# Optimization experiments

Measured on AMD Instinct MI355X. Metric: run time of the kernel, lower is better.

The kernel has to match this reference:

```python
import jax, jax.numpy as jnp
import numpy as np

INPUT_SZ, HIDDEN_SZ, OUTPUT_SZ, NUM_LAYERS, EMBED_SZ = 128, 512, 64, 4, 16
SEQ_LEN, BATCH = 128, 256


def setup_inputs() -> dict:
    key = jax.random.key(0)
    ks = jax.random.split(key, 12)
    H, E, L = HIDDEN_SZ, EMBED_SZ, NUM_LAYERS
    s = 0.05
    inp = {
        "input": jax.random.randint(ks[0], (SEQ_LEN, BATCH), 0, INPUT_SZ),
        "embed": jax.random.normal(ks[1], (INPUT_SZ, E), jnp.float32) * s,
        # layer 0 (input dim = E), dims: [dir=2, 4H, in]
        "Wih0": jax.random.normal(ks[2], (2, 4 * H, E), jnp.float32) * s,
        "Whh0": jax.random.normal(ks[3], (2, 4 * H, H), jnp.float32) * s,
        "bih0": jax.random.normal(ks[4], (2, 4 * H), jnp.float32) * s,
        "bhh0": jax.random.normal(ks[5], (2, 4 * H), jnp.float32) * s,
        # layers 1..L-1 (input dim = 2H)
        "Wih": jax.random.normal(ks[6], (L - 1, 2, 4 * H, 2 * H), jnp.float32) * s,
        "Whh": jax.random.normal(ks[7], (L - 1, 2, 4 * H, H), jnp.float32) * s,
        "bih": jax.random.normal(ks[8], (L - 1, 2, 4 * H), jnp.float32) * s,
        "bhh": jax.random.normal(ks[9], (L - 1, 2, 4 * H), jnp.float32) * s,
        "fc_w": jax.random.normal(ks[10], (OUTPUT_SZ, 4 * L * H), jnp.float32) * s,
        "fc_b": jax.random.normal(ks[11], (OUTPUT_SZ,), jnp.float32) * s,
    }
    return inp


def _lstm_forward(tokens, embed, Wih0, Whh0, bih0, bhh0, Wih, Whh, bih, bhh, fc_w, fc_b):
    L, H = NUM_LAYERS, HIDDEN_SZ
    T, B = tokens.shape
    xs = embed[tokens]  # [T, B, E]

    def step(carry, x_t):
        h, c = carry  # each [L, 2, B, H]
        x = x_t       # [B, in_dim]
        new_h, new_c = [], []
        for l in range(L):
            Wi = Wih0 if l == 0 else Wih[l - 1]
            Wh = Whh0 if l == 0 else Whh[l - 1]
            b = (bih0 + bhh0) if l == 0 else (bih[l - 1] + bhh[l - 1])
            # both directions see the same single-timestep input (PyTorch
            # bidirectional LSTM called with seq_len=1 per step)
            gates = (jnp.einsum('bi,dgi->dbg', x, Wi)
                     + jnp.einsum('dbh,dgh->dbg', h[l], Wh)
                     + b[:, None, :])  # [2, B, 4H]
            i_g, f_g, g_g, o_g = jnp.split(gates, 4, axis=-1)
            c_new = jax.nn.sigmoid(f_g) * c[l] + jax.nn.sigmoid(i_g) * jnp.tanh(g_g)
            h_new = jax.nn.sigmoid(o_g) * jnp.tanh(c_new)  # [2, B, H]
            new_h.append(h_new)
            new_c.append(c_new)
            x = jnp.concatenate([h_new[0], h_new[1]], axis=-1)  # [B, 2H]
        return (jnp.stack(new_h), jnp.stack(new_c)), None

    h0 = jnp.zeros((L, 2, B, H), xs.dtype)
    c0 = jnp.zeros((L, 2, B, H), xs.dtype)
    (h, c), _ = jax.lax.scan(step, (h0, c0), xs)

    # PyTorch layout: [2L, B, H], layer-major / direction-minor
    h = h.reshape(2 * L, B, H)
    c = c.reshape(2 * L, B, H)
    hid = jnp.concatenate([h, c], axis=2)                 # [2L, B, 2H]
    hid = hid.transpose(1, 0, 2).reshape(B, 4 * L * H)    # cat over 2L slices on dim 1
    out = hid @ fc_w.T + fc_b
    # dropout is identity at inference
    return jax.nn.softmax(out, axis=1)


def reference(input, embed, Wih0, Whh0, bih0, bhh0, Wih, Whh, bih, bhh, fc_w, fc_b):
    return _lstm_forward(input, embed, Wih0, Whh0, bih0, bhh0, Wih, Whh, bih, bhh, fc_w, fc_b)
```

## Files before the change

### kernel.cpp

```cpp
#include <hip/hip_runtime.h>

using short8 = __attribute__((ext_vector_type(8))) short;
using f32x4  = __attribute__((ext_vector_type(4))) float;

static constexpr size_t N_WF0 = (size_t)2*32*8*3*4*512;
static constexpr size_t N_WF1 = (size_t)6*32*8*6*4*512;
static constexpr size_t N_WF  = N_WF0 + N_WF1;
static constexpr size_t N_BSE = (size_t)8*2048;
static constexpr size_t N_XPE = (size_t)128*2*256*8;
static constexpr size_t N_HBE = (size_t)2*8*64*256*8;
static constexpr size_t N_CBE = (size_t)8*256*512;
static constexpr size_t N_FCT = (size_t)8192*64;
static constexpr size_t N_FL  = (size_t)8*128;

static constexpr size_t OFF_WF = 0;
static constexpr size_t OFF_BS = OFF_WF + N_WF*2;
static constexpr size_t OFF_XP = OFF_BS + N_BSE*4;
static constexpr size_t OFF_HB = OFF_XP + N_XPE*2;
static constexpr size_t OFF_CB = OFF_HB + N_HBE*2;
static constexpr size_t OFF_HF = OFF_CB + N_CBE*4;
static constexpr size_t OFF_FC = OFF_HF + N_CBE*4;
static constexpr size_t OFF_FL = OFF_FC + N_FCT*4;
static constexpr size_t WS_NEEDED = OFF_FL + N_FL*4;

static constexpr int LDS_A   = 2*8*6*1024;
static constexpr int LDS_RED = 8*4*16*20*4;
static constexpr int LDS_C   = 16*256*4;
static constexpr int LDS_TOT = LDS_A + LDS_RED + LDS_C;

__device__ __forceinline__ short f2bf(float f) {
  unsigned u = __float_as_uint(f);
  u += 0x7fff + ((u >> 16) & 1);
  return (short)(u >> 16);
}

__device__ __forceinline__ void wait_ge(int* f, int target) {
  while (__hip_atomic_load(f, __ATOMIC_RELAXED, __HIP_MEMORY_SCOPE_SYSTEM) < target)
    __builtin_amdgcn_s_sleep(1);
}

__device__ __forceinline__ void dma16(const void* g, void* l) {
  __builtin_amdgcn_global_load_lds((const __attribute__((address_space(1))) unsigned int*)g,
                                   (__attribute__((address_space(3))) unsigned int*)l, 16, 0, 17);
}

__device__ __forceinline__ void lds_barrier() {
  __builtin_amdgcn_sched_barrier(0);
  __builtin_amdgcn_s_waitcnt(0xC07F);
  __builtin_amdgcn_s_barrier();
  __builtin_amdgcn_sched_barrier(0);
}

__global__ void k_prep_wf(const float* __restrict__ Wih0, const float* __restrict__ Whh0,
                          const float* __restrict__ Wih,  const float* __restrict__ Whh,
                          short* __restrict__ Wf) {
  size_t idx = (size_t)blockIdx.x * blockDim.x + threadIdx.x;
  if (idx >= N_WF) return;
  int j  = (int)(idx & 7);
  int lane = (int)((idx >> 3) & 63);
  int gt = (int)((idx >> 9) & 3);
  int lr = lane & 15, qq = lane >> 4;
  float v;
  if (idx < N_WF0) {
    size_t rest = idx >> 11;
    int sl = (int)(rest % 3); size_t r2 = rest / 3;
    int wvv = (int)(r2 & 7);  size_t r3 = r2 >> 3;
    int ncc = (int)(r3 & 31); int dd = (int)(r3 >> 5);
    int g = gt*512 + ncc*16 + lr;
    int k = (wvv*3 + sl)*32 + qq*8 + j;
    if (k < 16)       v = Wih0[((size_t)dd*2048 + g)*16 + k];
    else if (k < 64)  v = 0.f;
    else if (k < 576) v = Whh0[((size_t)dd*2048 + g)*512 + (k - 64)];
    else              v = 0.f;
  } else {
    size_t u = idx - N_WF0;
    size_t rest = u >> 11;
    int sl = (int)(rest % 6); size_t r2 = rest / 6;
    int wvv = (int)(r2 & 7);  size_t r3 = r2 >> 3;
    int ncc = (int)(r3 & 31); int ldm = (int)(r3 >> 5);
    int g = gt*512 + ncc*16 + lr;
    int k = (wvv*6 + sl)*32 + qq*8 + j;
    if (k < 1024) v = Wih[((size_t)ldm*2048 + g)*1024 + k];
    else          v = Whh[((size_t)ldm*2048 + g)*512 + (k - 1024)];
  }
  Wf[idx] = f2bf(v);
}

__global__ void k_prep_bias(const float* __restrict__ bih0, const float* __restrict__ bhh0,
                            const float* __restrict__ bih, const float* __restrict__ bhh,
                            float* __restrict__ bsum) {
  int idx = blockIdx.x * blockDim.x + threadIdx.x;
  if (idx >= (int)N_BSE) return;
  int g = idx & 2047;
  int dd = (idx >> 11) & 1;
  int ll = idx >> 12;
  float v;
  if (ll == 0) v = bih0[dd*2048 + g] + bhh0[dd*2048 + g];
  else         v = bih[((ll-1)*2 + dd)*2048 + g] + bhh[((ll-1)*2 + dd)*2048 + g];
  bsum[idx] = v;
}

__global__ void k_prep_xp(const int* __restrict__ tok, const float* __restrict__ embed,
                          short* __restrict__ XP) {
  int idx = blockIdx.x * blockDim.x + threadIdx.x;
  if (idx >= (int)N_XPE) return;
  int i  = idx & 7;
  int b  = (idx >> 3) & 255;
  int kg = (idx >> 11) & 1;
  int t  = idx >> 12;
  int k = kg*8 + i;
  XP[idx] = f2bf(embed[tok[t*256 + b]*16 + k]);
}

__global__ void k_prep_fcT(const float* __restrict__ fc_w, float* __restrict__ fcT) {
  int idx = blockIdx.x * blockDim.x + threadIdx.x;
  if (idx >= (int)N_FCT) return;
  int o = idx & 63;
  int k = idx >> 6;
  fcT[idx] = fc_w[o * 8192 + k];
}

__global__ void __launch_bounds__(512, 2)
k_lstm(const short* __restrict__ Wf, const float* __restrict__ bsum,
       const short* __restrict__ XP, short* __restrict__ hb,
       float* __restrict__ cF, float* __restrict__ hf, int* __restrict__ Fl) {
  extern __shared__ char smem[];
  char*  As  = smem;
  float* red = (float*)(smem + LDS_A);
  float* cL  = (float*)(smem + LDS_A + LDS_RED);

  const int blk = blockIdx.x;
  const int ld = blk & 7, nc = blk >> 3;
  const int l = ld >> 1, d = ld & 1;
  const int tid = threadIdx.x;
  const int wv = tid >> 6, lane = tid & 63;
  const int q = lane >> 4, lr = lane & 15;
  const int li = lane & 15, lk = lane >> 4;
  const int SL = (l == 0) ? 3 : 6;
  const int SUMW = (l == 0) ? 6 : 8;
  const bool act = (l > 0) || (wv < 6);
  const size_t HB_LD = 131072;

  for (int i = tid; i < 4096; i += 512) cL[i] = 0.f;

  float b4[4];
  if (tid < 256) {
    int en = tid & 15;
    #pragma unroll
    for (int gt = 0; gt < 4; ++gt)
      b4[gt] = bsum[ld*2048 + gt*512 + nc*16 + en];
  }

  short8 wreg[6][4];
  {
    const short* wb = (l == 0)
      ? (Wf + (size_t)(d*32 + nc) * (8*3*4*512) + (size_t)wv * (3*4*512))
      : (Wf + N_WF0 + (size_t)((ld - 2)*32 + nc) * (8*6*4*512) + (size_t)wv * (6*4*512));
    #pragma unroll
    for (int sl = 0; sl < 6; ++sl) {
      #pragma unroll
      for (int gt = 0; gt < 4; ++gt) {
        if (sl < SL) wreg[sl][gt] = *(const short8*)(wb + (sl*4 + gt)*512 + lane*8);
        else         wreg[sl][gt] = short8{0,0,0,0,0,0,0,0};
      }
    }
  }
  __syncthreads();

  for (int t = 0; t < 128; ++t) {
    if (tid == 0 && t > 0)           wait_ge(Fl + ld*128 + (t-1), 32);
    if (tid == 1 && l > 0)           wait_ge(Fl + (ld-2-d)*128 + t, 32);
    if (tid == 2 && l > 0)           wait_ge(Fl + (ld-1-d)*128 + t, 32);
    if (tid == 3 && l < 3 && t >= 2) wait_ge(Fl + (2*l+2)*128 + (t-2), 32);
    if (tid == 4 && l < 3 && t >= 2) wait_ge(Fl + (2*l+3)*128 + (t-2), 32);
    __syncthreads();

    const int pt = t & 1, pm = pt ^ 1;

    const short* apl[6];
    #pragma unroll
    for (int sl = 0; sl < 6; ++sl) {
      if (sl < SL && act) {
        int S = wv * SL + sl;
        const short* p;
        if (l == 0) {
          if (S < 2) p = XP + (size_t)t*4096 + (size_t)(lk & 1)*2048;
          else       p = hb + (size_t)(pm*8 + ld)*HB_LD + (size_t)(4*S - 8 + lk)*2048;
        } else {
          const int pl0 = ld - 2 - d;
          if (S < 16)      p = hb + (size_t)(pt*8 + pl0    )*HB_LD + (size_t)(4*S       + lk)*2048;
          else if (S < 32) p = hb + (size_t)(pt*8 + pl0 + 1)*HB_LD + (size_t)(4*S - 64  + lk)*2048;
          else             p = hb + (size_t)(pm*8 + ld     )*HB_LD + (size_t)(4*S - 128 + lk)*2048;
        }
        apl[sl] = p + li*8;
      } else apl[sl] = nullptr;
    }

    if (act) {
      #pragma unroll
      for (int sl = 0; sl < 6; ++sl)
        if (sl < SL) dma16(apl[sl], As + ((0*8 + wv)*6 + sl)*1024);
    }

    for (int ro = 0; ro < 16; ++ro) {
      if (act && ro < 15) {
        #pragma unroll
        for (int sl = 0; sl < 6; ++sl)
          if (sl < SL) dma16(apl[sl] + (ro+1)*128, As + ((((ro+1)&1)*8 + wv)*6 + sl)*1024);
      }
      __builtin_amdgcn_sched_barrier(0);
      if (act) {
        if (ro < 15) { if (l == 0) __builtin_amdgcn_s_waitcnt(0xF73);
                       else        __builtin_amdgcn_s_waitcnt(0xF76); }
        else         __builtin_amdgcn_s_waitcnt(0xF70);
      }
      __builtin_amdgcn_sched_barrier(0);

      if (act) {
        const char* ab = As + (size_t)(((ro&1)*8 + wv)*6)*1024 + (size_t)lane*16;
        f32x4 acc[4];
        #pragma unroll
        for (int gt = 0; gt < 4; ++gt) acc[gt] = f32x4{0.f,0.f,0.f,0.f};
        #pragma unroll
        for (int sl = 0; sl < 6; ++sl)
          if (sl < SL) {
            short8 af = *(const short8*)(ab + sl*1024);
            #pragma unroll
            for (int gt = 0; gt < 4; ++gt)
              acc[gt] = __builtin_amdgcn_mfma_f32_16x16x32_bf16(af, wreg[sl][gt], acc[gt], 0,0,0);
          }
        #pragma unroll
        for (int gt = 0; gt < 4; ++gt)
          *(f32x4*)&red[(((wv*4 + gt)*16) + lr)*20 + q*4] = acc[gt];
      }
      lds_barrier();

      if (tid < 256) {
        const int m  = tid >> 4;
        const int en = tid & 15;
        const int j  = nc*16 + en;
        const int b  = ro*16 + m;
        float g4[4];
        #pragma unroll
        for (int gt = 0; gt < 4; ++gt) {
          float s = 0.f;
          for (int w = 0; w < SUMW; ++w)
            s += red[((w*4 + gt)*16 + en)*20 + m];
          g4[gt] = s + b4[gt];
        }
        float cold = cL[ro*256 + tid];
        float si = 1.f/(1.f + __expf(-g4[0]));
        float sf = 1.f/(1.f + __expf(-g4[1]));
        float so = 1.f/(1.f + __expf(-g4[3]));
        float tg = 1.f - 2.f/(1.f + __expf(2.f*g4[2]));
        float cn = sf * cold + si * tg;
        float tc = 1.f - 2.f/(1.f + __expf(2.f*cn));
        float hn = so * tc;
        cL[ro*256 + tid] = cn;
        short* hw = hb + (size_t)(pt*8 + ld)*HB_LD;
        __hip_atomic_store(&hw[((size_t)(j >> 3)*256 + b)*8 + (j & 7)], f2bf(hn),
                           __ATOMIC_RELAXED, __HIP_MEMORY_SCOPE_SYSTEM);
        if (t == 127) {
          hf[((size_t)ld*256 + b)*512 + j] = hn;
          cF[((size_t)ld*256 + b)*512 + j] = cn;
        }
      }
      if (ro < 15) lds_barrier();
      else         __syncthreads();
    }

    if (tid == 0)
      __hip_atomic_fetch_add(Fl + ld*128 + t, 1, __ATOMIC_RELAXED, __HIP_MEMORY_SCOPE_SYSTEM);
  }
}

__global__ void __launch_bounds__(256)
k_fc(const float* __restrict__ hf, const float* __restrict__ cb,
     const float* __restrict__ fcT, const float* __restrict__ fc_b,
     float* __restrict__ out) {
  const int tid = threadIdx.x;
  const int o = tid & 63;
  const int qw = tid >> 6;
  const int bi = blockIdx.x * 4 + qw;
  __shared__ float hidc[4][128];
  float acc = 0.f;
  for (int k0 = 0; k0 < 8192; k0 += 128) {
    #pragma unroll
    for (int c = 0; c < 2; ++c) {
      int idx = tid + c * 256;
      int r = idx >> 7, kk = idx & 127;
      int k = k0 + kk;
      int sS = k >> 10, rem = k & 1023, part = rem >> 9, j = rem & 511;
      const float* src = part ? cb : hf;
      hidc[r][kk] = src[((size_t)sS * 256 + (blockIdx.x * 4 + r)) * 512 + j];
    }
    __syncthreads();
    const float* hrow = hidc[qw];
    #pragma unroll 8
    for (int kk = 0; kk < 128; ++kk)
      acc += hrow[kk] * fcT[(size_t)(k0 + kk) * 64 + o];
    __syncthreads();
  }
  float v = acc + fc_b[o];
  float m = v;
  #pragma unroll
  for (int off = 32; off; off >>= 1) m = fmaxf(m, __shfl_xor(m, off, 64));
  float e = __expf(v - m);
  float ssum = e;
  #pragma unroll
  for (int off = 32; off; off >>= 1) ssum += __shfl_xor(ssum, off, 64);
  out[bi * 64 + o] = e / ssum;
}

extern "C" void kernel_launch(void* const* d_in, const int* in_sizes, int n_in,
                              void* d_out, int out_size, void* d_ws, size_t ws_size,
                              hipStream_t stream) {
  const int*   tok   = (const int*)d_in[0];
  const float* embed = (const float*)d_in[1];
  const float* Wih0  = (const float*)d_in[2];
  const float* Whh0  = (const float*)d_in[3];
  const float* bih0  = (const float*)d_in[4];
  const float* bhh0  = (const float*)d_in[5];
  const float* Wih   = (const float*)d_in[6];
  const float* Whh   = (const float*)d_in[7];
  const float* bih   = (const float*)d_in[8];
  const float* bhh   = (const float*)d_in[9];
  const float* fc_w  = (const float*)d_in[10];
  const float* fc_b  = (const float*)d_in[11];
  float* out = (float*)d_out;

  if (ws_size < WS_NEEDED) return;

  char* ws = (char*)d_ws;
  short* Wfb  = (short*)(ws + OFF_WF);
  float* bsum = (float*)(ws + OFF_BS);
  short* XP   = (short*)(ws + OFF_XP);
  short* hbuf = (short*)(ws + OFF_HB);
  float* cFb  = (float*)(ws + OFF_CB);
  float* hfb  = (float*)(ws + OFF_HF);
  float* fcT  = (float*)(ws + OFF_FC);
  int*   flg  = (int*)  (ws + OFF_FL);

  hipMemsetAsync(ws + OFF_HB + N_HBE, 0, N_HBE, stream);
  hipMemsetAsync(ws + OFF_FL, 0, N_FL * 4, stream);

  k_prep_wf  <<<(int)((N_WF  + 255) / 256), 256, 0, stream>>>(Wih0, Whh0, Wih, Whh, Wfb);
  k_prep_bias<<<(int)((N_BSE + 255) / 256), 256, 0, stream>>>(bih0, bhh0, bih, bhh, bsum);
  k_prep_xp  <<<(int)((N_XPE + 255) / 256), 256, 0, stream>>>(tok, embed, XP);
  k_prep_fcT <<<(int)((N_FCT + 255) / 256), 256, 0, stream>>>(fc_w, fcT);

  (void)hipFuncSetAttribute((const void*)k_lstm,
                            hipFuncAttributeMaxDynamicSharedMemorySize, LDS_TOT);

  void* kargs[] = {(void*)&Wfb, (void*)&bsum, (void*)&XP,
                   (void*)&hbuf, (void*)&cFb, (void*)&hfb, (void*)&flg};
  hipLaunchCooperativeKernel((void*)k_lstm, dim3(256), dim3(512), kargs, LDS_TOT, stream);

  k_fc<<<64, 256, 0, stream>>>(hfb, cFb, fcT, fc_b, out);
}
```

Baseline: 5.706 ms.

## Stage layer inputs into per-layer local buffers and relax DMA cache policy

Each layer>0 block now copies its slice of the previous layer's hidden state from the shared hb buffer into a per-(layer,direction) double-buffered xl buffer. An extra intra-layer flag barrier (Fi) makes every block of the layer wait until all slices are staged. Own hidden state is also written into xl, so global_load_lds reads come from this buffer with a cache policy of 1 (0 for the token embeddings) instead of 17. The intent is better cache locality for the recurrent reads and fewer system-scope coherent loads. The cost is an extra copy and an extra grid-level wait per timestep, plus retuned waitcnt values that carry a risk of being wrong.

Result: slower. 6.488 ms (+13.7%).

```diff
diff --git a/kernel.cpp b/kernel.cpp
--- a/kernel.cpp
+++ b/kernel.cpp
@@ -12,6 +12,9 @@
 static constexpr size_t N_CBE = (size_t)8*256*512;
 static constexpr size_t N_FCT = (size_t)8192*64;
 static constexpr size_t N_FL  = (size_t)8*128;
+static constexpr size_t XL_LD = (size_t)192*2048;
+static constexpr size_t N_XLE = (size_t)16*XL_LD;
+static constexpr size_t N_FIE = (size_t)8*128;
 
 static constexpr size_t OFF_WF = 0;
 static constexpr size_t OFF_BS = OFF_WF + N_WF*2;
@@ -21,7 +24,9 @@
 static constexpr size_t OFF_HF = OFF_CB + N_CBE*4;
 static constexpr size_t OFF_FC = OFF_HF + N_CBE*4;
 static constexpr size_t OFF_FL = OFF_FC + N_FCT*4;
-static constexpr size_t WS_NEEDED = OFF_FL + N_FL*4;
+static constexpr size_t OFF_XL = OFF_FL + N_FL*4;
+static constexpr size_t OFF_FI = OFF_XL + N_XLE*2;
+static constexpr size_t WS_NEEDED = OFF_FI + N_FIE*4;
 
 static constexpr int LDS_A   = 2*8*6*1024;
 static constexpr int LDS_RED = 8*4*16*20*4;
@@ -39,9 +44,13 @@
     __builtin_amdgcn_s_sleep(1);
 }
 
-__device__ __forceinline__ void dma16(const void* g, void* l) {
+__device__ __forceinline__ void dma16c(const void* g, void* l) {
   __builtin_amdgcn_global_load_lds((const __attribute__((address_space(1))) unsigned int*)g,
-                                   (__attribute__((address_space(3))) unsigned int*)l, 16, 0, 17);
+                                   (__attribute__((address_space(3))) unsigned int*)l, 16, 0, 1);
+}
+__device__ __forceinline__ void dma16x(const void* g, void* l) {
+  __builtin_amdgcn_global_load_lds((const __attribute__((address_space(1))) unsigned int*)g,
+                                   (__attribute__((address_space(3))) unsigned int*)l, 16, 0, 0);
 }
 
 __device__ __forceinline__ void lds_barrier() {
@@ -123,7 +132,8 @@
 __global__ void __launch_bounds__(512, 2)
 k_lstm(const short* __restrict__ Wf, const float* __restrict__ bsum,
        const short* __restrict__ XP, short* __restrict__ hb,
-       float* __restrict__ cF, float* __restrict__ hf, int* __restrict__ Fl) {
+       short* __restrict__ xl, float* __restrict__ cF, float* __restrict__ hf,
+       int* __restrict__ Fl, int* __restrict__ Fi) {
   extern __shared__ char smem[];
   char*  As  = smem;
   float* red = (float*)(smem + LDS_A);
@@ -139,6 +149,7 @@
   const int SL = (l == 0) ? 3 : 6;
   const int SUMW = (l == 0) ? 6 : 8;
   const bool act = (l > 0) || (wv < 6);
+  const int selfb = (l == 0) ? 0 : 128;
   const size_t HB_LD = 131072;
 
   for (int i = tid; i < 4096; i += 512) cL[i] = 0.f;
@@ -176,43 +187,76 @@
     __syncthreads();
 
     const int pt = t & 1, pm = pt ^ 1;
+    const short* xlp = xl + ((size_t)ld*2 + pt)*XL_LD;
+    const short* xlm = xl + ((size_t)ld*2 + pm)*XL_LD;
+
+    if (l > 0) {
+      const int pl0 = ld - 2 - d;
+      const int* s0 = (const int*)(hb + (size_t)(pt*8 + pl0    )*HB_LD);
+      const int* s1 = (const int*)(hb + (size_t)(pt*8 + pl0 + 1)*HB_LD);
+      int* dst = (int*)(xl + ((size_t)ld*2 + pt)*XL_LD);
+      #pragma unroll
+      for (int i = 0; i < 8; ++i) {
+        int dw = tid + i*512;
+        int kga = nc*4 + (dw >> 10);
+        int off = dw & 1023;
+        int v = (kga < 64)
+          ? __hip_atomic_load(s0 + (size_t)kga*1024 + off, __ATOMIC_RELAXED, __HIP_MEMORY_SCOPE_SYSTEM)
+          : __hip_atomic_load(s1 + (size_t)(kga-64)*1024 + off, __ATOMIC_RELAXED, __HIP_MEMORY_SCOPE_SYSTEM);
+        dst[(size_t)kga*1024 + off] = v;
+      }
+      __syncthreads();
+      if (tid == 5) {
+        __hip_atomic_fetch_add(Fi + ld*128 + t, 1, __ATOMIC_RELAXED, __HIP_MEMORY_SCOPE_SYSTEM);
+        wait_ge(Fi + ld*128 + t, 32);
+      }
+      __syncthreads();
+    }
 
     const short* apl[6];
+    bool xp_slab[6];
     #pragma unroll
     for (int sl = 0; sl < 6; ++sl) {
+      apl[sl] = nullptr; xp_slab[sl] = false;
       if (sl < SL && act) {
         int S = wv * SL + sl;
-        const short* p;
         if (l == 0) {
-          if (S < 2) p = XP + (size_t)t*4096 + (size_t)(lk & 1)*2048;
-          else       p = hb + (size_t)(pm*8 + ld)*HB_LD + (size_t)(4*S - 8 + lk)*2048;
+          if (S < 2) { apl[sl] = XP + (size_t)t*4096 + (size_t)(lk & 1)*2048 + li*8; xp_slab[sl] = true; }
+          else         apl[sl] = xlm + (size_t)(4*S - 8 + lk)*2048 + li*8;
         } else {
-          const int pl0 = ld - 2 - d;
-          if (S < 16)      p = hb + (size_t)(pt*8 + pl0    )*HB_LD + (size_t)(4*S       + lk)*2048;
-          else if (S < 32) p = hb + (size_t)(pt*8 + pl0 + 1)*HB_LD + (size_t)(4*S - 64  + lk)*2048;
-          else             p = hb + (size_t)(pm*8 + ld     )*HB_LD + (size_t)(4*S - 128 + lk)*2048;
+          const short* base = (S < 32) ? xlp : xlm;
+          apl[sl] = base + (size_t)(4*S + lk)*2048 + li*8;
         }
-        apl[sl] = p + li*8;
-      } else apl[sl] = nullptr;
+      }
     }
 
     if (act) {
       #pragma unroll
       for (int sl = 0; sl < 6; ++sl)
-        if (sl < SL) dma16(apl[sl], As + ((0*8 + wv)*6 + sl)*1024);
+        if (sl < SL) {
+          if (xp_slab[sl]) dma16x(apl[sl], As + ((0*8 + wv)*6 + sl)*1024);
+          else             dma16c(apl[sl], As + ((0*8 + wv)*6 + sl)*1024);
+        }
     }
 
     for (int ro = 0; ro < 16; ++ro) {
       if (act && ro < 15) {
         #pragma unroll
         for (int sl = 0; sl < 6; ++sl)
-          if (sl < SL) dma16(apl[sl] + (ro+1)*128, As + ((((ro+1)&1)*8 + wv)*6 + sl)*1024);
+          if (sl < SL) {
+            if (xp_slab[sl]) dma16x(apl[sl] + (ro+1)*128, As + ((((ro+1)&1)*8 + wv)*6 + sl)*1024);
+            else             dma16c(apl[sl] + (ro+1)*128, As + ((((ro+1)&1)*8 + wv)*6 + sl)*1024);
+          }
       }
       __builtin_amdgcn_sched_barrier(0);
       if (act) {
-        if (ro < 15) { if (l == 0) __builtin_amdgcn_s_waitcnt(0xF73);
-                       else        __builtin_amdgcn_s_waitcnt(0xF76); }
-        else         __builtin_amdgcn_s_waitcnt(0xF70);
+        if (ro == 0)       { if (l == 0) __builtin_amdgcn_s_waitcnt(0xF73);
+                             else        __builtin_amdgcn_s_waitcnt(0xF76); }
+        else if (ro < 15)  { if (l == 0) __builtin_amdgcn_s_waitcnt(0xF75);
+                             else if (l < 3) __builtin_amdgcn_s_waitcnt(0xF78);
+                             else            __builtin_amdgcn_s_waitcnt(0xF77); }
+        else               { if (l == 3) __builtin_amdgcn_s_waitcnt(0xF71);
+                             else        __builtin_amdgcn_s_waitcnt(0xF72); }
       }
       __builtin_amdgcn_sched_barrier(0);
 
@@ -257,9 +301,14 @@
         float tc = 1.f - 2.f/(1.f + __expf(2.f*cn));
         float hn = so * tc;
         cL[ro*256 + tid] = cn;
-        short* hw = hb + (size_t)(pt*8 + ld)*HB_LD;
-        __hip_atomic_store(&hw[((size_t)(j >> 3)*256 + b)*8 + (j & 7)], f2bf(hn),
-                           __ATOMIC_RELAXED, __HIP_MEMORY_SCOPE_SYSTEM);
+        short hbf = f2bf(hn);
+        short* xw = (short*)(xl + ((size_t)ld*2 + pt)*XL_LD);
+        xw[((size_t)(selfb + (j >> 3))*256 + b)*8 + (j & 7)] = hbf;
+        if (l < 3) {
+          short* hw = hb + (size_t)(pt*8 + ld)*HB_LD;
+          __hip_atomic_store(&hw[((size_t)(j >> 3)*256 + b)*8 + (j & 7)], hbf,
+                             __ATOMIC_RELAXED, __HIP_MEMORY_SCOPE_SYSTEM);
+        }
         if (t == 127) {
           hf[((size_t)ld*256 + b)*512 + j] = hn;
           cF[((size_t)ld*256 + b)*512 + j] = cn;
@@ -340,9 +389,12 @@
   float* hfb  = (float*)(ws + OFF_HF);
   float* fcT  = (float*)(ws + OFF_FC);
   int*   flg  = (int*)  (ws + OFF_FL);
-
-  hipMemsetAsync(ws + OFF_HB + N_HBE, 0, N_HBE, stream);
+  short* xlb  = (short*)(ws + OFF_XL);
+  int*   fim  = (int*)  (ws + OFF_FI);
+
   hipMemsetAsync(ws + OFF_FL, 0, N_FL * 4, stream);
+  hipMemsetAsync(ws + OFF_FI, 0, N_FIE * 4, stream);
+  hipMemsetAsync(ws + OFF_XL, 0, N_XLE * 2, stream);
 
   k_prep_wf  <<<(int)((N_WF  + 255) / 256), 256, 0, stream>>>(Wih0, Whh0, Wih, Whh, Wfb);
   k_prep_bias<<<(int)((N_BSE + 255) / 256), 256, 0, stream>>>(bih0, bhh0, bih, bhh, bsum);
@@ -352,8 +404,8 @@
   (void)hipFuncSetAttribute((const void*)k_lstm,
                             hipFuncAttributeMaxDynamicSharedMemorySize, LDS_TOT);
 
-  void* kargs[] = {(void*)&Wfb, (void*)&bsum, (void*)&XP,
-                   (void*)&hbuf, (void*)&cFb, (void*)&hfb, (void*)&flg};
+  void* kargs[] = {(void*)&Wfb, (void*)&bsum, (void*)&XP, (void*)&hbuf,
+                   (void*)&xlb, (void*)&cFb, (void*)&hfb, (void*)&flg, (void*)&fim};
   hipLaunchCooperativeKernel((void*)k_lstm, dim3(256), dim3(512), kargs, LDS_TOT, stream);
 
   k_fc<<<64, 256, 0, stream>>>(hfb, cFb, fcT, fc_b, out);
```
